# Performance work log

Hardware: AMD Instinct MI355X
Metric: run time of the kernel (lower is better)

The kernel has to match this reference:

```python
import jax, jax.numpy as jnp
import numpy as np

B, N, D, H = 2, 2048, 1024, 16
HD = D // H  # head dim = 64
SCALING = (D / H) ** 0.5  # sqrt(64) = 8
EPS = 1e-5


def setup_inputs() -> dict:
    key = jax.random.key(0)
    k1, k2, k3 = jax.random.split(key, 3)
    return {
        "z": jax.random.normal(k1, (B, N, D), dtype=jnp.float32),
        "ln_scale": jnp.ones((D,), dtype=jnp.float32),
        "ln_bias": jnp.zeros((D,), dtype=jnp.float32),
        "w_qkv": jax.random.normal(k2, (D, 3 * D), dtype=jnp.float32) * (D ** -0.5),
        "w_proj": jax.random.normal(k3, (D, D), dtype=jnp.float32) * (D ** -0.5),
        "b_proj": jnp.zeros((D,), dtype=jnp.float32),
    }


def reference(z, ln_scale, ln_bias, w_qkv, w_proj, b_proj):
    b, n, d = z.shape
    # LayerNorm (pre-norm)
    mu = jnp.mean(z, axis=-1, keepdims=True)
    var = jnp.mean(jnp.square(z - mu), axis=-1, keepdims=True)
    zn = (z - mu) / jnp.sqrt(var + EPS) * ln_scale + ln_bias
    # QKV projection: [b, n, 3D]
    qkv = zn @ w_qkv
    # einops 'b n (h d qkv_n) -> qkv_n b h n d': qkv index is innermost
    qkv5 = qkv.reshape(b, n, H, HD, 3)  # [b, n, h, d, 3]
    q = jnp.transpose(qkv5[..., 0], (0, 2, 1, 3))  # [b, h, n, d]
    k = jnp.transpose(qkv5[..., 1], (0, 2, 1, 3))
    v = jnp.transpose(qkv5[..., 2], (0, 2, 1, 3))
    # Attention: scores scaled AFTER the matmul, as in the source
    scores = jnp.einsum('bhqd,bhkd->bhqk', q, k) / SCALING
    att = jax.nn.softmax(scores, axis=-1)
    out = jnp.einsum('bhal,bhlv->bhav', att, v)  # [b, h, n, d]
    out = jnp.transpose(out, (0, 2, 1, 3)).reshape(b, n, d)  # merge heads
    out = out @ w_proj + b_proj  # projection (dropout p=0)
    return z + out
```

## Files before the change

### kernel.cpp

```cpp
#include <hip/hip_runtime.h>
#include <stdint.h>
#include <math.h>

typedef unsigned short u16;
typedef float f32x4 __attribute__((ext_vector_type(4)));
typedef __bf16 bf16x8 __attribute__((ext_vector_type(8)));

__device__ __forceinline__ u16 f2bf(float f) {
    union { float f; uint32_t u; } c; c.f = f;
    return (u16)((c.u + 0x7FFFu + ((c.u >> 16) & 1u)) >> 16);
}

__device__ __forceinline__ void gload_lds16(const void* g, void* l) {
    __builtin_amdgcn_global_load_lds(
        (const __attribute__((address_space(1))) unsigned int*)g,
        (__attribute__((address_space(3))) unsigned int*)l, 16, 0, 0);
}

__global__ __launch_bounds__(256) void prep_kernel(const float* __restrict__ z,
                                                   const float* __restrict__ sc,
                                                   const float* __restrict__ bs,
                                                   const float* __restrict__ w_qkv,
                                                   const float* __restrict__ w_proj,
                                                   u16* __restrict__ zn,
                                                   u16* __restrict__ wqkvT,
                                                   u16* __restrict__ wprojT) {
    __shared__ float t[32][33];
    const int tid = threadIdx.x;
    const int bid = blockIdx.x;

    if (bid < 4096) {
        float* red = &t[0][0];
        const int row = bid;
        const float4 v = ((const float4*)(z + (size_t)row * 1024))[tid];
        float s = v.x + v.y + v.z + v.w;
        #pragma unroll
        for (int off = 32; off > 0; off >>= 1) s += __shfl_xor(s, off);
        if ((tid & 63) == 0) red[tid >> 6] = s;
        __syncthreads();
        const float mean = (red[0] + red[1] + red[2] + red[3]) * (1.0f / 1024.0f);
        const float dx = v.x - mean, dy = v.y - mean, dz = v.z - mean, dw = v.w - mean;
        float q = dx * dx + dy * dy + dz * dz + dw * dw;
        #pragma unroll
        for (int off = 32; off > 0; off >>= 1) q += __shfl_xor(q, off);
        if ((tid & 63) == 0) red[4 + (tid >> 6)] = q;
        __syncthreads();
        const float var = (red[4] + red[5] + red[6] + red[7]) * (1.0f / 1024.0f);
        const float rstd = rsqrtf(var + 1e-5f);
        const float4 scv = ((const float4*)sc)[tid];
        const float4 bsv = ((const float4*)bs)[tid];
        const u16 o0 = f2bf(dx * rstd * scv.x + bsv.x);
        const u16 o1 = f2bf(dy * rstd * scv.y + bsv.y);
        const u16 o2 = f2bf(dz * rstd * scv.z + bsv.z);
        const u16 o3 = f2bf(dw * rstd * scv.w + bsv.w);
        uint2 pk;
        pk.x = (uint32_t)o0 | ((uint32_t)o1 << 16);
        pk.y = (uint32_t)o2 | ((uint32_t)o3 << 16);
        *(uint2*)&zn[(size_t)row * 1024 + tid * 4] = pk;
        return;
    }

    const float* in;
    u16* out;
    int K, N, permute, bx, by;
    if (bid < 4096 + 3072) {
        const int r = bid - 4096;
        in = w_qkv; out = wqkvT; K = 1024; N = 3072; permute = 1;
        bx = r % 96; by = r / 96;
    } else {
        const int r = bid - 4096 - 3072;
        in = w_proj; out = wprojT; K = 1024; N = 1024; permute = 0;
        bx = r % 32; by = r / 32;
    }
    const int j = tid & 31, i0 = tid >> 5;
    const int kb = by * 32, nb = bx * 32;
    #pragma unroll
    for (int p = 0; p < 4; ++p) {
        int r = i0 + p * 8;
        t[r][j] = in[(size_t)(kb + r) * N + nb + j];
    }
    __syncthreads();
    #pragma unroll
    for (int p = 0; p < 4; ++p) {
        int r = i0 + p * 8;
        int c = nb + r;
        int np = c;
        if (permute) {
            int h = c / 192, rem = c - h * 192;
            int d = rem / 3, s = rem - d * 3;
            np = s * 1024 + h * 64 + d;
        }
        out[(size_t)np * K + kb + j] = f2bf(t[j][r]);
    }
}

__global__ __launch_bounds__(256, 3) void gemm_qkv(const u16* __restrict__ A,
                                                   const u16* __restrict__ Bt,
                                                   u16* __restrict__ qbuf,
                                                   u16* __restrict__ kbuf,
                                                   u16* __restrict__ vT) {
    __shared__ __align__(16) u16 sm[64 * 136];
    u16* const As = sm;
    u16* const Bs = sm + 4096;
    const int tid = threadIdx.x;
    const int wave = tid >> 6, lane = tid & 63;
    const int quad = lane >> 4, l16 = lane & 15;
    const int wm = (wave >> 1) * 64, wn = (wave & 1) * 64;
    const int row0 = blockIdx.x * 128, col0 = blockIdx.y * 128;
    const int gr = lane >> 2, gc = (lane & 3) * 8;
    f32x4 acc[4][4] = {};
    for (int kt = 0; kt < 1024; kt += 32) {
        __syncthreads();
        #pragma unroll
        for (int i = 0; i < 2; ++i) {
            const int rb = wave * 16 + i * 64;
            gload_lds16(&A[(size_t)(row0 + rb + gr) * 1024 + kt + gc], &As[rb * 32]);
            gload_lds16(&Bt[(size_t)(col0 + rb + gr) * 1024 + kt + gc], &Bs[rb * 32]);
        }
        __syncthreads();
        bf16x8 ax[4], bx[4];
        #pragma unroll
        for (int t = 0; t < 4; ++t) {
            ax[t] = *(const bf16x8*)&As[(wm + t * 16 + l16) * 32 + quad * 8];
            bx[t] = *(const bf16x8*)&Bs[(wn + t * 16 + l16) * 32 + quad * 8];
        }
        #pragma unroll
        for (int mt = 0; mt < 4; ++mt)
            #pragma unroll
            for (int nt = 0; nt < 4; ++nt)
                acc[mt][nt] = __builtin_amdgcn_mfma_f32_16x16x32_bf16(ax[mt], bx[nt], acc[mt][nt], 0, 0, 0);
    }
    const int s = col0 >> 10;
    if (s < 2) {
        u16* const dst = (s == 0) ? qbuf : kbuf;
        const float scl = (s == 0) ? 0.125f * 1.44269504088896f : 1.0f;
        #pragma unroll
        for (int mt = 0; mt < 4; ++mt) {
            #pragma unroll
            for (int nt = 0; nt < 4; ++nt) {
                #pragma unroll
                for (int e = 0; e < 4; ++e) {
                    const int row = row0 + wm + mt * 16 + quad * 4 + e;
                    const int col = col0 + wn + nt * 16 + l16;
                    const int b = row >> 11, n = row & 2047;
                    const int h = (col >> 6) & 15, d = col & 63;
                    dst[((size_t)(b * 16 + h) * 2048 + n) * 64 + d] = f2bf(acc[mt][nt][e] * scl);
                }
            }
        }
    } else {
        const int b = row0 >> 11, n0 = row0 & 2047;
        const int h0 = (col0 >> 6) & 15;
        for (int hh = 0; hh < 2; ++hh) {
            __syncthreads();
            if ((wave & 1) == hh) {
                #pragma unroll
                for (int mt = 0; mt < 4; ++mt) {
                    const int rl = wm + mt * 16 + quad * 4;
                    #pragma unroll
                    for (int nt = 0; nt < 4; ++nt) {
                        const int cl = nt * 16 + l16;
                        u16 tmp[4];
                        #pragma unroll
                        for (int e = 0; e < 4; ++e) tmp[e] = f2bf(acc[mt][nt][e]);
                        *(uint2*)&sm[cl * 136 + rl] = *(const uint2*)tmp;
                    }
                }
            }
            __syncthreads();
            const int bh = b * 16 + h0 + hh;
            #pragma unroll
            for (int pass = 0; pass < 4; ++pass) {
                const int chunk = pass * 256 + tid;
                const int d = chunk >> 4;
                const int nc = chunk & 15;
                const uint4 vv = *(const uint4*)&sm[d * 136 + nc * 8];
                *(uint4*)&vT[((size_t)bh * 64 + d) * 2048 + n0 + nc * 8] = vv;
            }
        }
    }
}

__global__ __launch_bounds__(256, 2) void attn_kernel(const u16* __restrict__ qb,
                                                      const u16* __restrict__ kb,
                                                      const u16* __restrict__ vT,
                                                      u16* __restrict__ att_out) {
    __shared__ __align__(16) u16 smem[2][16384];
    const int tid = threadIdx.x;
    const int wave = tid >> 6, lane = tid & 63;
    const int quad = lane >> 4, l16 = lane & 15;
    const int qt = blockIdx.x, bh = blockIdx.y;
    const int b = bh >> 4, h = bh & 15;

    const u16* qrowA = &qb[(size_t)(bh * 2048 + qt * 128 + wave * 32 + l16) * 64];
    const bf16x8 qA0 = *(const bf16x8*)&qrowA[quad * 8];
    const bf16x8 qA1 = *(const bf16x8*)&qrowA[32 + quad * 8];
    const u16* qrowB = qrowA + 16 * 64;
    const bf16x8 qB0 = *(const bf16x8*)&qrowB[quad * 8];
    const bf16x8 qB1 = *(const bf16x8*)&qrowB[32 + quad * 8];

    const u16* ksrc[4];
    const u16* vsrc[4];
    int kofs[4], vofs[4];
    #pragma unroll
    for (int j = 0; j < 4; ++j) {
        const int p = 8 * wave + 32 * j + (lane >> 3);
        const int kr = (p & 0x60) | ((p & 12) << 1) | ((p & 16) >> 2) | (p & 3);
        const int gk = (lane & 7) ^ (p & 7);
        ksrc[j] = kb + ((size_t)bh * 2048 + kr) * 64 + gk * 8;
        kofs[j] = (8 * wave + 32 * j) * 64;
        const int d = 4 * wave + 16 * j + (lane >> 4);
        const int gv = (lane & 15) ^ (d & 15);
        vsrc[j] = vT + ((size_t)bh * 64 + d) * 2048 + gv * 8;
        vofs[j] = 8192 + (4 * wave + 16 * j) * 128;
    }

    f32x4 oA[4] = {}, oB[4] = {};
    f32x4 lA = {}, lB = {};
    bf16x8 ones;
    #pragma unroll
    for (int i = 0; i < 8; ++i) ones[i] = (__bf16)1.0f;

    #pragma unroll
    for (int j = 0; j < 4; ++j) {
        gload_lds16(ksrc[j], &smem[0][kofs[j]]);
        gload_lds16(vsrc[j], &smem[0][vofs[j]]);
        ksrc[j] += 128 * 64;
        vsrc[j] += 128;
    }

    for (int kt = 0; kt < 16; ++kt) {
        __syncthreads();
        if (kt < 15) {
            u16* nb_ = smem[(kt + 1) & 1];
            #pragma unroll
            for (int j = 0; j < 4; ++j) {
                gload_lds16(ksrc[j], &nb_[kofs[j]]);
                gload_lds16(vsrc[j], &nb_[vofs[j]]);
                ksrc[j] += 128 * 64;
                vsrc[j] += 128;
            }
        }
        const u16* Ks = smem[kt & 1];
        const u16* Vs = smem[kt & 1] + 8192;

        f32x4 sA[8] = {}, sB[8] = {};
        __builtin_amdgcn_s_setprio(1);
        #pragma unroll
        for (int nt = 0; nt < 8; ++nt) {
            const int r = nt * 16 + l16;
            const bf16x8 k0 = *(const bf16x8*)&Ks[r * 64 + (((quad) ^ (r & 7)) << 3)];
            const bf16x8 k1 = *(const bf16x8*)&Ks[r * 64 + (((quad + 4) ^ (r & 7)) << 3)];
            sA[nt] = __builtin_amdgcn_mfma_f32_16x16x32_bf16(k0, qA0, sA[nt], 0, 0, 0);
            sA[nt] = __builtin_amdgcn_mfma_f32_16x16x32_bf16(k1, qA1, sA[nt], 0, 0, 0);
            sB[nt] = __builtin_amdgcn_mfma_f32_16x16x32_bf16(k0, qB0, sB[nt], 0, 0, 0);
            sB[nt] = __builtin_amdgcn_mfma_f32_16x16x32_bf16(k1, qB1, sB[nt], 0, 0, 0);
        }
        __builtin_amdgcn_s_setprio(0);

        bf16x8 apA[4], apB[4];
        #pragma unroll
        for (int nt = 0; nt < 8; ++nt) {
            #pragma unroll
            for (int e = 0; e < 4; ++e) {
                apA[nt >> 1][(nt & 1) * 4 + e] = (__bf16)__builtin_amdgcn_exp2f(sA[nt][e]);
                apB[nt >> 1][(nt & 1) * 4 + e] = (__bf16)__builtin_amdgcn_exp2f(sB[nt][e]);
            }
        }

        __builtin_amdgcn_s_setprio(1);
        #pragma unroll
        for (int vt = 0; vt < 4; ++vt) {
            const int dd = vt * 16 + l16;
            #pragma unroll
            for (int c = 0; c < 4; ++c) {
                const bf16x8 vf = *(const bf16x8*)&Vs[dd * 128 + (((c * 4 + quad) ^ l16) << 3)];
                oA[vt] = __builtin_amdgcn_mfma_f32_16x16x32_bf16(apA[c], vf, oA[vt], 0, 0, 0);
                oB[vt] = __builtin_amdgcn_mfma_f32_16x16x32_bf16(apB[c], vf, oB[vt], 0, 0, 0);
            }
        }
        #pragma unroll
        for (int c = 0; c < 4; ++c) {
            lA = __builtin_amdgcn_mfma_f32_16x16x32_bf16(apA[c], ones, lA, 0, 0, 0);
            lB = __builtin_amdgcn_mfma_f32_16x16x32_bf16(apB[c], ones, lB, 0, 0, 0);
        }
        __builtin_amdgcn_s_setprio(0);
    }

    #pragma unroll
    for (int e = 0; e < 4; ++e) {
        const float invA = 1.0f / lA[e];
        const float invB = 1.0f / lB[e];
        const int nA = qt * 128 + wave * 32 + quad * 4 + e;
        #pragma unroll
        for (int vt = 0; vt < 4; ++vt) {
            att_out[(size_t)(b * 2048 + nA) * 1024 + h * 64 + vt * 16 + l16] = f2bf(oA[vt][e] * invA);
            att_out[(size_t)(b * 2048 + nA + 16) * 1024 + h * 64 + vt * 16 + l16] = f2bf(oB[vt][e] * invB);
        }
    }
}

__global__ __launch_bounds__(256) void gemm_proj(const u16* __restrict__ A,
                                                 const u16* __restrict__ Bt,
                                                 const float* __restrict__ bias,
                                                 const float* __restrict__ z,
                                                 float* __restrict__ out) {
    __shared__ __align__(16) u16 As[64 * 32];
    __shared__ __align__(16) u16 Bs[128 * 32];
    const int tid = threadIdx.x;
    const int wave = tid >> 6, lane = tid & 63;
    const int quad = lane >> 4, l16 = lane & 15;
    const int wm = (wave >> 1) * 32, wn = (wave & 1) * 64;
    const int row0 = blockIdx.x * 64, col0 = blockIdx.y * 128;
    const int gr = lane >> 2, gc = (lane & 3) * 8;
    f32x4 acc[2][4] = {};
    for (int kt = 0; kt < 1024; kt += 32) {
        __syncthreads();
        gload_lds16(&A[(size_t)(row0 + wave * 16 + gr) * 1024 + kt + gc], &As[(wave * 16) * 32]);
        #pragma unroll
        for (int i = 0; i < 2; ++i) {
            const int rb = wave * 16 + i * 64;
            gload_lds16(&Bt[(size_t)(col0 + rb + gr) * 1024 + kt + gc], &Bs[rb * 32]);
        }
        __syncthreads();
        bf16x8 ax[2], bx[4];
        #pragma unroll
        for (int t = 0; t < 2; ++t)
            ax[t] = *(const bf16x8*)&As[(wm + t * 16 + l16) * 32 + quad * 8];
        #pragma unroll
        for (int t = 0; t < 4; ++t)
            bx[t] = *(const bf16x8*)&Bs[(wn + t * 16 + l16) * 32 + quad * 8];
        #pragma unroll
        for (int mt = 0; mt < 2; ++mt)
            #pragma unroll
            for (int nt = 0; nt < 4; ++nt)
                acc[mt][nt] = __builtin_amdgcn_mfma_f32_16x16x32_bf16(ax[mt], bx[nt], acc[mt][nt], 0, 0, 0);
    }
    #pragma unroll
    for (int mt = 0; mt < 2; ++mt) {
        #pragma unroll
        for (int nt = 0; nt < 4; ++nt) {
            #pragma unroll
            for (int e = 0; e < 4; ++e) {
                const int row = row0 + wm + mt * 16 + quad * 4 + e;
                const int col = col0 + wn + nt * 16 + l16;
                out[(size_t)row * 1024 + col] = acc[mt][nt][e] + bias[col] + z[(size_t)row * 1024 + col];
            }
        }
    }
}

extern "C" void kernel_launch(void* const* d_in, const int* in_sizes, int n_in,
                              void* d_out, int out_size, void* d_ws, size_t ws_size,
                              hipStream_t stream) {
    const float* z        = (const float*)d_in[0];
    const float* ln_scale = (const float*)d_in[1];
    const float* ln_bias  = (const float*)d_in[2];
    const float* w_qkv    = (const float*)d_in[3];
    const float* w_proj   = (const float*)d_in[4];
    const float* b_proj   = (const float*)d_in[5];
    float* out = (float*)d_out;

    char* ws = (char*)d_ws;
    u16* zn     = (u16*)(ws);
    u16* wqkvT  = (u16*)(ws + (8u << 20));
    u16* wprojT = (u16*)(ws + (14u << 20));
    u16* qbuf   = (u16*)(ws + (16u << 20));
    u16* kbuf   = (u16*)(ws + (24u << 20));
    u16* vT     = (u16*)(ws + (32u << 20));
    u16* att_o  = (u16*)(ws + (40u << 20));

    prep_kernel<<<dim3(4096 + 3072 + 1024), 256, 0, stream>>>(
        z, ln_scale, ln_bias, w_qkv, w_proj, zn, wqkvT, wprojT);
    gemm_qkv<<<dim3(32, 24), 256, 0, stream>>>(zn, wqkvT, qbuf, kbuf, vT);
    attn_kernel<<<dim3(16, 32), 256, 0, stream>>>(qbuf, kbuf, vT, att_o);
    gemm_proj<<<dim3(64, 8), 256, 0, stream>>>(att_o, wprojT, b_proj, z, out);
}
```

Measured before the change: 177.6 us.

## Split attention key tiles across waves with cross-wave LDS reduction

The attention block grows to 512 threads (8 waves). Waves are split into 2 query groups × 4 key-slices, and each wave handles 64 query rows against a 32-key slice of every 128-key tile instead of all keys for 32 rows. Partial outputs and row sums are reduced through LDS at the end, before normalisation and bf16 store. This reuses K/V fragments across more query rows per wave and adds waves for latency hiding, at the cost of a larger LDS footprint (70KB), an extra reduction phase, and more accumulator registers per wave.

```diff
diff --git a/kernel.cpp b/kernel.cpp
--- a/kernel.cpp
+++ b/kernel.cpp
@@ -181,50 +181,53 @@
     }
 }
 
-__global__ __launch_bounds__(256, 2) void attn_kernel(const u16* __restrict__ qb,
+__global__ __launch_bounds__(512, 2) void attn_kernel(const u16* __restrict__ qb,
                                                       const u16* __restrict__ kb,
                                                       const u16* __restrict__ vT,
                                                       u16* __restrict__ att_out) {
-    __shared__ __align__(16) u16 smem[2][16384];
+    __shared__ __align__(16) char lds_raw[71680];
+    u16* const smem0 = (u16*)lds_raw;
     const int tid = threadIdx.x;
     const int wave = tid >> 6, lane = tid & 63;
     const int quad = lane >> 4, l16 = lane & 15;
+    const int kw = wave & 3, qw = wave >> 2;
     const int qt = blockIdx.x, bh = blockIdx.y;
     const int b = bh >> 4, h = bh & 15;
 
-    const u16* qrowA = &qb[(size_t)(bh * 2048 + qt * 128 + wave * 32 + l16) * 64];
-    const bf16x8 qA0 = *(const bf16x8*)&qrowA[quad * 8];
-    const bf16x8 qA1 = *(const bf16x8*)&qrowA[32 + quad * 8];
-    const u16* qrowB = qrowA + 16 * 64;
-    const bf16x8 qB0 = *(const bf16x8*)&qrowB[quad * 8];
-    const bf16x8 qB1 = *(const bf16x8*)&qrowB[32 + quad * 8];
-
-    const u16* ksrc[4];
-    const u16* vsrc[4];
-    int kofs[4], vofs[4];
-    #pragma unroll
-    for (int j = 0; j < 4; ++j) {
-        const int p = 8 * wave + 32 * j + (lane >> 3);
+    bf16x8 qf[4][2];
+    #pragma unroll
+    for (int g = 0; g < 4; ++g) {
+        const u16* qrow = &qb[(size_t)(bh * 2048 + qt * 128 + qw * 64 + g * 16 + l16) * 64];
+        qf[g][0] = *(const bf16x8*)&qrow[quad * 8];
+        qf[g][1] = *(const bf16x8*)&qrow[32 + quad * 8];
+    }
+
+    const u16* ksrc[2];
+    const u16* vsrc[2];
+    int kofs[2], vofs[2];
+    #pragma unroll
+    for (int j = 0; j < 2; ++j) {
+        const int p = 8 * wave + 64 * j + (lane >> 3);
         const int kr = (p & 0x60) | ((p & 12) << 1) | ((p & 16) >> 2) | (p & 3);
         const int gk = (lane & 7) ^ (p & 7);
         ksrc[j] = kb + ((size_t)bh * 2048 + kr) * 64 + gk * 8;
-        kofs[j] = (8 * wave + 32 * j) * 64;
-        const int d = 4 * wave + 16 * j + (lane >> 4);
+        kofs[j] = (8 * wave + 64 * j) * 64;
+        const int d = 4 * wave + 32 * j + (lane >> 4);
         const int gv = (lane & 15) ^ (d & 15);
         vsrc[j] = vT + ((size_t)bh * 64 + d) * 2048 + gv * 8;
-        vofs[j] = 8192 + (4 * wave + 16 * j) * 128;
-    }
-
-    f32x4 oA[4] = {}, oB[4] = {};
-    f32x4 lA = {}, lB = {};
+        vofs[j] = 8192 + (4 * wave + 32 * j) * 128;
+    }
+
+    f32x4 o[4][4] = {};
+    f32x4 l[4] = {};
     bf16x8 ones;
     #pragma unroll
     for (int i = 0; i < 8; ++i) ones[i] = (__bf16)1.0f;
 
     #pragma unroll
-    for (int j = 0; j < 4; ++j) {
-        gload_lds16(ksrc[j], &smem[0][kofs[j]]);
-        gload_lds16(vsrc[j], &smem[0][vofs[j]]);
+    for (int j = 0; j < 2; ++j) {
+        gload_lds16(ksrc[j], smem0 + kofs[j]);
+        gload_lds16(vsrc[j], smem0 + vofs[j]);
         ksrc[j] += 128 * 64;
         vsrc[j] += 128;
     }
@@ -232,70 +235,94 @@
     for (int kt = 0; kt < 16; ++kt) {
         __syncthreads();
         if (kt < 15) {
-            u16* nb_ = smem[(kt + 1) & 1];
-            #pragma unroll
-            for (int j = 0; j < 4; ++j) {
-                gload_lds16(ksrc[j], &nb_[kofs[j]]);
-                gload_lds16(vsrc[j], &nb_[vofs[j]]);
+            u16* nb_ = smem0 + ((kt + 1) & 1) * 16384;
+            #pragma unroll
+            for (int j = 0; j < 2; ++j) {
+                gload_lds16(ksrc[j], nb_ + kofs[j]);
+                gload_lds16(vsrc[j], nb_ + vofs[j]);
                 ksrc[j] += 128 * 64;
                 vsrc[j] += 128;
             }
         }
-        const u16* Ks = smem[kt & 1];
-        const u16* Vs = smem[kt & 1] + 8192;
-
-        f32x4 sA[8] = {}, sB[8] = {};
+        const u16* Ks = smem0 + (kt & 1) * 16384;
+        const u16* Vs = Ks + 8192;
+
+        f32x4 s[2][4] = {};
         __builtin_amdgcn_s_setprio(1);
         #pragma unroll
-        for (int nt = 0; nt < 8; ++nt) {
-            const int r = nt * 16 + l16;
+        for (int mtl = 0; mtl < 2; ++mtl) {
+            const int r = kw * 32 + mtl * 16 + l16;
             const bf16x8 k0 = *(const bf16x8*)&Ks[r * 64 + (((quad) ^ (r & 7)) << 3)];
             const bf16x8 k1 = *(const bf16x8*)&Ks[r * 64 + (((quad + 4) ^ (r & 7)) << 3)];
-            sA[nt] = __builtin_amdgcn_mfma_f32_16x16x32_bf16(k0, qA0, sA[nt], 0, 0, 0);
-            sA[nt] = __builtin_amdgcn_mfma_f32_16x16x32_bf16(k1, qA1, sA[nt], 0, 0, 0);
-            sB[nt] = __builtin_amdgcn_mfma_f32_16x16x32_bf16(k0, qB0, sB[nt], 0, 0, 0);
-            sB[nt] = __builtin_amdgcn_mfma_f32_16x16x32_bf16(k1, qB1, sB[nt], 0, 0, 0);
+            #pragma unroll
+            for (int g = 0; g < 4; ++g) {
+                s[mtl][g] = __builtin_amdgcn_mfma_f32_16x16x32_bf16(k0, qf[g][0], s[mtl][g], 0, 0, 0);
+                s[mtl][g] = __builtin_amdgcn_mfma_f32_16x16x32_bf16(k1, qf[g][1], s[mtl][g], 0, 0, 0);
+            }
         }
         __builtin_amdgcn_s_setprio(0);
 
-        bf16x8 apA[4], apB[4];
-        #pragma unroll
-        for (int nt = 0; nt < 8; ++nt) {
-            #pragma unroll
-            for (int e = 0; e < 4; ++e) {
-                apA[nt >> 1][(nt & 1) * 4 + e] = (__bf16)__builtin_amdgcn_exp2f(sA[nt][e]);
-                apB[nt >> 1][(nt & 1) * 4 + e] = (__bf16)__builtin_amdgcn_exp2f(sB[nt][e]);
-            }
-        }
+        bf16x8 ap[4];
+        #pragma unroll
+        for (int g = 0; g < 4; ++g)
+            #pragma unroll
+            for (int mtl = 0; mtl < 2; ++mtl)
+                #pragma unroll
+                for (int e = 0; e < 4; ++e)
+                    ap[g][mtl * 4 + e] = (__bf16)__builtin_amdgcn_exp2f(s[mtl][g][e]);
 
         __builtin_amdgcn_s_setprio(1);
         #pragma unroll
         for (int vt = 0; vt < 4; ++vt) {
             const int dd = vt * 16 + l16;
-            #pragma unroll
-            for (int c = 0; c < 4; ++c) {
-                const bf16x8 vf = *(const bf16x8*)&Vs[dd * 128 + (((c * 4 + quad) ^ l16) << 3)];
-                oA[vt] = __builtin_amdgcn_mfma_f32_16x16x32_bf16(apA[c], vf, oA[vt], 0, 0, 0);
-                oB[vt] = __builtin_amdgcn_mfma_f32_16x16x32_bf16(apB[c], vf, oB[vt], 0, 0, 0);
-            }
-        }
-        #pragma unroll
-        for (int c = 0; c < 4; ++c) {
-            lA = __builtin_amdgcn_mfma_f32_16x16x32_bf16(apA[c], ones, lA, 0, 0, 0);
-            lB = __builtin_amdgcn_mfma_f32_16x16x32_bf16(apB[c], ones, lB, 0, 0, 0);
-        }
+            const bf16x8 vf = *(const bf16x8*)&Vs[dd * 128 + (((kw * 4 + quad) ^ l16) << 3)];
+            #pragma unroll
+            for (int g = 0; g < 4; ++g)
+                o[g][vt] = __builtin_amdgcn_mfma_f32_16x16x32_bf16(ap[g], vf, o[g][vt], 0, 0, 0);
+        }
+        #pragma unroll
+        for (int g = 0; g < 4; ++g)
+            l[g] = __builtin_amdgcn_mfma_f32_16x16x32_bf16(ap[g], ones, l[g], 0, 0, 0);
         __builtin_amdgcn_s_setprio(0);
     }
 
-    #pragma unroll
-    for (int e = 0; e < 4; ++e) {
-        const float invA = 1.0f / lA[e];
-        const float invB = 1.0f / lB[e];
-        const int nA = qt * 128 + wave * 32 + quad * 4 + e;
-        #pragma unroll
-        for (int vt = 0; vt < 4; ++vt) {
-            att_out[(size_t)(b * 2048 + nA) * 1024 + h * 64 + vt * 16 + l16] = f2bf(oA[vt][e] * invA);
-            att_out[(size_t)(b * 2048 + nA + 16) * 1024 + h * 64 + vt * 16 + l16] = f2bf(oB[vt][e] * invB);
+    float* const red = (float*)lds_raw;
+    float* const lred = (float*)(lds_raw + 69632);
+    #pragma unroll
+    for (int qg = 0; qg < 2; ++qg) {
+        __syncthreads();
+        if (qw == qg) {
+            #pragma unroll
+            for (int g = 0; g < 4; ++g) {
+                #pragma unroll
+                for (int vt = 0; vt < 4; ++vt)
+                    #pragma unroll
+                    for (int e = 0; e < 4; ++e)
+                        red[(kw * 64 + g * 16 + quad * 4 + e) * 68 + vt * 16 + l16] = o[g][vt][e];
+                if (l16 == 0) {
+                    #pragma unroll
+                    for (int e = 0; e < 4; ++e)
+                        lred[kw * 64 + g * 16 + quad * 4 + e] = l[g][e];
+                }
+            }
+        }
+        __syncthreads();
+        #pragma unroll
+        for (int rep = 0; rep < 2; ++rep) {
+            const int idx = rep * 512 + tid;
+            const int q = idx >> 4, dc = idx & 15;
+            const f32x4 a0 = *(const f32x4*)&red[(0 * 64 + q) * 68 + dc * 4];
+            const f32x4 a1 = *(const f32x4*)&red[(1 * 64 + q) * 68 + dc * 4];
+            const f32x4 a2 = *(const f32x4*)&red[(2 * 64 + q) * 68 + dc * 4];
+            const f32x4 a3 = *(const f32x4*)&red[(3 * 64 + q) * 68 + dc * 4];
+            const f32x4 ss = a0 + a1 + a2 + a3;
+            const float li = lred[q] + lred[64 + q] + lred[128 + q] + lred[192 + q];
+            const float inv = 1.0f / li;
+            u16 pk[4];
+            #pragma unroll
+            for (int e = 0; e < 4; ++e) pk[e] = f2bf(ss[e] * inv);
+            const int qrow = qt * 128 + qg * 64 + q;
+            *(uint2*)&att_out[(size_t)(b * 2048 + qrow) * 1024 + h * 64 + dc * 4] = *(const uint2*)pk;
         }
     }
 }
@@ -373,6 +400,6 @@
     prep_kernel<<<dim3(4096 + 3072 + 1024), 256, 0, stream>>>(
         z, ln_scale, ln_bias, w_qkv, w_proj, zn, wqkvT, wprojT);
     gemm_qkv<<<dim3(32, 24), 256, 0, stream>>>(zn, wqkvT, qbuf, kbuf, vT);
-    attn_kernel<<<dim3(16, 32), 256, 0, stream>>>(qbuf, kbuf, vT, att_o);
+    attn_kernel<<<dim3(16, 32), 512, 0, stream>>>(qbuf, kbuf, vT, att_o);
     gemm_proj<<<dim3(64, 8), 256, 0, stream>>>(att_o, wprojT, b_proj, z, out);
 }
```

Result: no change. 180.3 us (+1.5%).
